# Performance work log

Hardware: AMD Instinct MI355X
Metric: run time of the kernel (lower is better)

The kernel has to match this reference:

```python
import jax, jax.numpy as jnp
import numpy as np

D_MODEL = 1024
NHEADS = 16
E_HEAD = D_MODEL // NHEADS  # 64
ROPE_BASE = 10000.0


def _rope_cos_sin(L, dim, base, dtype):
    # dim = E_head (even); inv_freq over pairs, GPT-NeoX half-split convention
    inv_freq = 1.0 / (base ** (jnp.arange(0, dim, 2, dtype=jnp.float32) / dim))
    pos = jnp.arange(L, dtype=jnp.float32)
    freqs = pos[:, None] * inv_freq[None, :]  # [L, dim/2]
    return jnp.cos(freqs).astype(dtype), jnp.sin(freqs).astype(dtype)


def _apply_rope(t, cos, sin):
    # t: [B, H, L, Dh]; rotate-half formulation
    d2 = t.shape[-1] // 2
    t1, t2 = t[..., :d2], t[..., d2:]
    return jnp.concatenate([t1 * cos - t2 * sin, t1 * sin + t2 * cos], axis=-1)


def setup_inputs() -> dict:
    key = jax.random.key(0)
    ks = jax.random.split(key, 5)
    B, L = 4, 2048
    x = jax.random.normal(ks[0], (B, L, D_MODEL), dtype=jnp.float32)
    s_in = 1.0 / np.sqrt(D_MODEL)
    W_packed = jax.random.normal(ks[1], (3 * D_MODEL, D_MODEL), dtype=jnp.float32) * s_in
    b_packed = jax.random.normal(ks[2], (3 * D_MODEL,), dtype=jnp.float32) * 0.02
    W_out = jax.random.normal(ks[3], (D_MODEL, D_MODEL), dtype=jnp.float32) * s_in
    b_out = jax.random.normal(ks[4], (D_MODEL,), dtype=jnp.float32) * 0.02
    return {"x": x, "W_packed": W_packed, "b_packed": b_packed, "W_out": W_out, "b_out": b_out}


def reference(x, W_packed, b_packed, W_out, b_out):
    B, L, _ = x.shape
    # 1) packed QKV projection (query is key is value path)
    qkv = jnp.einsum('ble,fe->blf', x, W_packed) + b_packed  # [B, L, 3*D]
    q, k, v = jnp.split(qkv, 3, axis=-1)
    # 2) split heads -> [B, H, L, Dh]
    def heads(t):
        return t.reshape(B, L, NHEADS, E_HEAD).transpose(0, 2, 1, 3)
    q, k, v = heads(q), heads(k), heads(v)
    # 3) RoPE on q, k
    cos, sin = _rope_cos_sin(L, E_HEAD, ROPE_BASE, x.dtype)
    q = _apply_rope(q, cos, sin)
    k = _apply_rope(k, cos, sin)
    # 4) SDPA (non-causal, no dropout)
    scale = 1.0 / np.sqrt(E_HEAD)
    scores = jnp.einsum('bhqd,bhkd->bhqk', q, k) * scale
    attn = jax.nn.softmax(scores, axis=-1)
    out = jnp.einsum('bhqk,bhkd->bhqd', attn, v)
    # 5) merge heads + output projection
    out = out.transpose(0, 2, 1, 3).reshape(B, L, D_MODEL)
    return jnp.einsum('bld,ed->ble', out, W_out) + b_out
```

## Files before the change

### kernel.cpp

```cpp
#include <hip/hip_runtime.h>
#include <hip/hip_bf16.h>
#include <stdint.h>

#define L_SEQ 2048
#define NB    4
#define NH    16
#define EH    64
#define DM    1024
#define MTOT  (NB * L_SEQ)

typedef __attribute__((ext_vector_type(8))) short bf16x8;
typedef __attribute__((ext_vector_type(4))) float f32x4;
typedef __attribute__((ext_vector_type(16))) float f32x16;
typedef __attribute__((ext_vector_type(2))) unsigned uint2v;

static __device__ __forceinline__ float bf2f(short u) {
    union { unsigned int i; float f; } c;
    c.i = ((unsigned int)(unsigned short)u) << 16;
    return c.f;
}
static __device__ __forceinline__ short f2bf(float f) {
    union { float f; unsigned int i; } c; c.f = f;
    unsigned int x = c.i;
    unsigned int r = (x + 0x7fffu + ((x >> 16) & 1u)) >> 16;
    return (short)(unsigned short)r;
}
static __device__ __forceinline__ unsigned cvtpk(float lo, float hi) {
    unsigned r;
    asm volatile("v_cvt_pk_bf16_f32 %0, %1, %2" : "=v"(r) : "v"(lo), "v"(hi));
    return r;
}
static __device__ __forceinline__ float pairsum(float x) {
    union { float f; unsigned u; } c; c.f = x;
    uint2v r = __builtin_amdgcn_permlane32_swap(c.u, c.u, false, false);
    union { unsigned u; float f; } a, b; a.u = r[0]; b.u = r[1];
    return a.f + b.f;
}

static __device__ __forceinline__ void gload_lds16(const void* g, void* lds) {
    __builtin_amdgcn_global_load_lds(
        (const __attribute__((address_space(1))) unsigned int*)g,
        (__attribute__((address_space(3))) unsigned int*)lds, 16, 0, 0);
}

__global__ __launch_bounds__(256) void cvt3_k(const float* __restrict__ x,
                                              const float* __restrict__ wp,
                                              const float* __restrict__ wo,
                                              short* __restrict__ xb,
                                              short* __restrict__ wpb,
                                              short* __restrict__ wob,
                                              float* __restrict__ tab) {
    int bid = blockIdx.x;
    if (bid >= 12288) {
        int i = (bid - 12288) * 256 + threadIdx.x;
        int l = i >> 5, d = i & 31;
        float inv = powf(10000.0f, -(float)d * (1.0f / 32.0f));
        float fr = (float)l * inv;
        tab[i]         = cosf(fr);
        tab[65536 + i] = sinf(fr);
        return;
    }
    const float* src; short* dst; int i;
    if (bid < 8192)       { src = x;  dst = xb;  i = bid * 256 + threadIdx.x; }
    else if (bid < 11264) { src = wp; dst = wpb; i = (bid - 8192) * 256 + threadIdx.x; }
    else                  { src = wo; dst = wob; i = (bid - 11264) * 256 + threadIdx.x; }
    float4 v = ((const float4*)src)[i];
    short4 o;
    o.x = f2bf(v.x); o.y = f2bf(v.y); o.z = f2bf(v.z); o.w = f2bf(v.w);
    ((short4*)dst)[i] = o;
}

template<int OUTBF16, int NBN, int NCOL, int EPI>
__global__ __launch_bounds__(512, 2) void gemmA_k(const short* __restrict__ A,
                                                  const short* __restrict__ Bt,
                                                  const float* __restrict__ bias,
                                                  void* __restrict__ Cv,
                                                  short* __restrict__ Qp,
                                                  short* __restrict__ Kp,
                                                  short* __restrict__ Vt,
                                                  const float* __restrict__ tab) {
    __shared__ short lds[3][384 * 32];
    const int t = threadIdx.x;
    const int w = t >> 6, l = t & 63;
    const int wm = w >> 1, wn = w & 1;
    const int lr = l & 15, lh = l >> 4;

    const int nblk = NBN * 32;
    int fid = blockIdx.x + blockIdx.y * NBN;
    int swz = (fid & 7) * (nblk >> 3) + (fid >> 3);
    const int n0 = (swz % NBN) * 128;
    const int m0 = (swz / NBN) * 256;

    const int lrow = l >> 2;
    const int schunk = (l & 3) ^ ((l >> 3) & 3);

    const short* Ag = A + (size_t)(m0 + lrow) * 1024 + schunk * 8;
    const short* Bg = Bt + (size_t)(n0 + lrow) * 1024 + schunk * 8;

    auto STAGE = [&](int kt, short* dst) {
        gload_lds16(Ag + (size_t)(w * 32) * 1024 + kt * 32,      dst + (w * 32) * 32);
        gload_lds16(Ag + (size_t)(w * 32 + 16) * 1024 + kt * 32, dst + (w * 32 + 16) * 32);
        gload_lds16(Bg + (size_t)(w * 16) * 1024 + kt * 32,      dst + 8192 + (w * 16) * 32);
    };

    f32x4 acc[4][4] = {};

    STAGE(0, &lds[0][0]);
    STAGE(1, &lds[1][0]);
    asm volatile("s_waitcnt vmcnt(3)" ::: "memory");
    __builtin_amdgcn_s_barrier();

    short* Pc = &lds[0][0];
    short* Pn = &lds[1][0];
    short* Pf = &lds[2][0];

    const int fch = (lh ^ ((lr >> 1) & 3)) << 3;

    for (int kt = 0; kt < 32; ++kt) {
        if (kt < 30) STAGE(kt + 2, Pf);

        const short* Al = Pc;
        const short* Bl = Pc + 8192;

        bf16x8 bfr[4], af[4];
#pragma unroll
        for (int nj = 0; nj < 4; ++nj)
            bfr[nj] = *(const bf16x8*)(Bl + (wn * 64 + nj * 16 + lr) * 32 + fch);
#pragma unroll
        for (int mi = 0; mi < 4; ++mi)
            af[mi] = *(const bf16x8*)(Al + (wm * 64 + mi * 16 + lr) * 32 + fch);

        __builtin_amdgcn_s_setprio(1);
#pragma unroll
        for (int mi = 0; mi < 4; ++mi)
#pragma unroll
            for (int nj = 0; nj < 4; ++nj)
                acc[mi][nj] = __builtin_amdgcn_mfma_f32_16x16x32_bf16(
                    af[mi], bfr[nj], acc[mi][nj], 0, 0, 0);
        __builtin_amdgcn_s_setprio(0);

        asm volatile("s_waitcnt lgkmcnt(0)" ::: "memory");
        if (kt < 30) asm volatile("s_waitcnt vmcnt(3)" ::: "memory");
        else         asm volatile("s_waitcnt vmcnt(0)" ::: "memory");
        __builtin_amdgcn_s_barrier();

        short* tp = Pc; Pc = Pn; Pn = Pf; Pf = tp;
    }

    if (EPI == 0) {
#pragma unroll
        for (int mi = 0; mi < 4; ++mi) {
#pragma unroll
            for (int nj = 0; nj < 4; ++nj) {
                const int row = m0 + wm * 64 + mi * 16 + lh * 4;
                const int col = n0 + wn * 64 + nj * 16 + lr;
                const float bsv = bias[col];
#pragma unroll
                for (int j = 0; j < 4; ++j) {
                    float v = acc[mi][nj][j] + bsv;
                    if (OUTBF16)
                        ((short*)Cv)[(size_t)(row + j) * NCOL + col] = f2bf(v);
                    else
                        ((float*)Cv)[(size_t)(row + j) * NCOL + col] = v;
                }
            }
        }
    } else {
        const int part = n0 >> 10;
        const int h = ((n0 & 1023) >> 6) + wn;
        if (part == 2) {
#pragma unroll
            for (int mi = 0; mi < 4; ++mi) {
                const int r0 = m0 + wm * 64 + mi * 16 + lh * 4;
                const int bq = r0 >> 11, lq = r0 & 2047;
                const int lpb = (lq & ~63) + (((mi * 2 + (lh & 1)) ^ (lr & 7)) << 3) + ((lh >> 1) * 4);
#pragma unroll
                for (int nj = 0; nj < 4; ++nj) {
                    const int d = nj * 16 + lr;
                    const float bsv = bias[n0 + wn * 64 + d];
                    short4 sv;
                    sv.x = f2bf(acc[mi][nj][0] + bsv);
                    sv.y = f2bf(acc[mi][nj][1] + bsv);
                    sv.z = f2bf(acc[mi][nj][2] + bsv);
                    sv.w = f2bf(acc[mi][nj][3] + bsv);
                    *(short4*)(Vt + (size_t)((bq * 16 + h) * 64 + d) * 2048 + lpb) = sv;
                }
            }
        } else {
            const float qsc = (part == 0) ? 0.18033688011112042f : 1.0f;
            short* Dst = (part == 0) ? Qp : Kp;
            const float b1l = bias[n0 + wn * 64 + lr];
            const float b1h = bias[n0 + wn * 64 + 16 + lr];
            const float b2l = bias[n0 + wn * 64 + 32 + lr];
            const float b2h = bias[n0 + wn * 64 + 48 + lr];
#pragma unroll
            for (int mi = 0; mi < 4; ++mi) {
                const int r0 = m0 + wm * 64 + mi * 16 + lh * 4;
                const int bq = r0 >> 11, lq0 = r0 & 2047;
                short* Drow = Dst + ((size_t)(bq * 16 + h) * 2048 + lq0) * 64;
#pragma unroll
                for (int j = 0; j < 4; ++j) {
                    const int ll = lq0 + j;
                    const int r7l = ll & 7;
#pragma unroll
                    for (int njl = 0; njl < 2; ++njl) {
                        const int d2 = njl * 16 + lr;
                        const float c = tab[ll * 32 + d2];
                        const float s = tab[65536 + ll * 32 + d2];
                        const float t1 = acc[mi][njl][j]     + (njl ? b1h : b1l);
                        const float t2 = acc[mi][njl + 2][j] + (njl ? b2h : b2l);
                        const float e1 = (t1 * c - t2 * s) * qsc;
                        const float e2 = (t1 * s + t2 * c) * qsc;
                        if (part == 0) {
                            Drow[j * 64 + d2]      = f2bf(e1);
                            Drow[j * 64 + d2 + 32] = f2bf(e2);
                        } else {
                            Drow[j * 64 + (((d2 >> 3) ^ r7l) * 8) + (d2 & 7)]       = f2bf(e1);
                            Drow[j * 64 + ((((d2 >> 3) | 4) ^ r7l) * 8) + (d2 & 7)] = f2bf(e2);
                        }
                    }
                }
            }
        }
    }
}

__global__ __launch_bounds__(512, 4) void attn_k(const short* __restrict__ Qg,
                                                 const short* __restrict__ Kg,
                                                 const short* __restrict__ Vt,
                                                 short* __restrict__ O) {
    __shared__ short Ks[3][64 * 64];
    __shared__ short Vs[3][64 * 64];
    const int t = threadIdx.x;
    const int w = t >> 6, l = t & 63;
    const int q = l & 31, hi = l >> 5;
    const int r7 = l & 7;

    const int od = blockIdx.x + blockIdx.y * 8;
    const int qblk = (od >> 3) & 7;
    const int bh = (od & 7) * 8 + (od >> 6);
    const int q0 = qblk * 256;

    const short* Qb = Qg + (size_t)bh * (2048 * 64);
    const short* Kb = Kg + (size_t)bh * (2048 * 64);
    const short* Vb = Vt + (size_t)bh * (64 * 2048);

    const int grow = w * 8 + (l >> 3);
    const int gcol = r7 * 8;

    gload_lds16(Kb + (size_t)grow * 64 + gcol,        &Ks[0][w * 512]);
    gload_lds16(Vb + (size_t)grow * 2048 + gcol,      &Vs[0][w * 512]);
    gload_lds16(Kb + (size_t)(64 + grow) * 64 + gcol, &Ks[1][w * 512]);
    gload_lds16(Vb + (size_t)grow * 2048 + 64 + gcol, &Vs[1][w * 512]);

    const int qrow = q0 + w * 32 + q;
    bf16x8 qf[4];
#pragma unroll
    for (int ds = 0; ds < 4; ds++)
        qf[ds] = *(const bf16x8*)(Qb + (size_t)qrow * 64 + ds * 16 + hi * 8);

    f32x16 o0 = {}, o1 = {};
    float lsumT = 0.0f;
    bf16x8 pf[4];

    asm volatile("s_waitcnt vmcnt(3)" ::: "memory");
    __builtin_amdgcn_s_barrier();

    {
        f32x16 s0 = {}, s1 = {};
#pragma unroll
        for (int ds = 0; ds < 4; ds++) {
            const int ch = ((ds << 1) | hi) ^ r7;
            bf16x8 k0f = *(const bf16x8*)(&Ks[0][0] + q * 64 + ch * 8);
            bf16x8 k1f = *(const bf16x8*)(&Ks[0][0] + (32 + q) * 64 + ch * 8);
            s0 = __builtin_amdgcn_mfma_f32_32x32x16_bf16(k0f, qf[ds], s0, 0, 0, 0);
            s1 = __builtin_amdgcn_mfma_f32_32x32x16_bf16(k1f, qf[ds], s1, 0, 0, 0);
        }
#pragma unroll
        for (int r = 0; r < 16; r++) {
            s0[r] = __builtin_amdgcn_exp2f(s0[r]);
            s1[r] = __builtin_amdgcn_exp2f(s1[r]);
        }
        float ts[16];
#pragma unroll
        for (int r = 0; r < 16; r++) ts[r] = s0[r] + s1[r];
#pragma unroll
        for (int st = 8; st >= 1; st >>= 1)
#pragma unroll
            for (int i = 0; i < 8; i++) if (i < st) ts[i] = ts[i] + ts[i + st];
        lsumT += pairsum(ts[0]);
        union { unsigned u[4]; bf16x8 v; } f;
        f.u[0] = cvtpk(s0[0], s0[1]);  f.u[1] = cvtpk(s0[2], s0[3]);
        f.u[2] = cvtpk(s0[4], s0[5]);  f.u[3] = cvtpk(s0[6], s0[7]);
        pf[0] = f.v;
        f.u[0] = cvtpk(s0[8], s0[9]);  f.u[1] = cvtpk(s0[10], s0[11]);
        f.u[2] = cvtpk(s0[12], s0[13]); f.u[3] = cvtpk(s0[14], s0[15]);
        pf[1] = f.v;
        f.u[0] = cvtpk(s1[0], s1[1]);  f.u[1] = cvtpk(s1[2], s1[3]);
        f.u[2] = cvtpk(s1[4], s1[5]);  f.u[3] = cvtpk(s1[6], s1[7]);
        pf[2] = f.v;
        f.u[0] = cvtpk(s1[8], s1[9]);  f.u[1] = cvtpk(s1[10], s1[11]);
        f.u[2] = cvtpk(s1[12], s1[13]); f.u[3] = cvtpk(s1[14], s1[15]);
        pf[3] = f.v;
    }

    asm volatile("s_waitcnt vmcnt(1)" ::: "memory");
    __builtin_amdgcn_s_barrier();

    const short* Kc = &Ks[0][0];  const short* Vc = &Vs[0][0];
    const short* Kn = &Ks[1][0];  const short* Vn = &Vs[1][0];
    short*       Kf = &Ks[2][0];  short*       Vf = &Vs[2][0];

    for (int it = 0; it < 32; ++it) {
        if (it < 30) {
            const int kn = (it + 2) * 64;
            gload_lds16(Kb + (size_t)(kn + grow) * 64 + gcol, Kf + w * 512);
            gload_lds16(Vb + (size_t)grow * 2048 + kn + gcol, Vf + w * 512);
        }

        f32x16 s0 = {}, s1 = {};
#pragma unroll
        for (int ks = 0; ks < 4; ks++) {
            const int ch = ((ks << 1) | hi) ^ r7;
            bf16x8 v0f = *(const bf16x8*)(Vc + q * 64 + ch * 8);
            bf16x8 v1f = *(const bf16x8*)(Vc + (32 + q) * 64 + ch * 8);
            __builtin_amdgcn_s_setprio(1);
            o0 = __builtin_amdgcn_mfma_f32_32x32x16_bf16(v0f, pf[ks], o0, 0, 0, 0);
            o1 = __builtin_amdgcn_mfma_f32_32x32x16_bf16(v1f, pf[ks], o1, 0, 0, 0);
            __builtin_amdgcn_s_setprio(0);
            if (it < 31) {
                bf16x8 k0f = *(const bf16x8*)(Kn + q * 64 + ch * 8);
                bf16x8 k1f = *(const bf16x8*)(Kn + (32 + q) * 64 + ch * 8);
                __builtin_amdgcn_s_setprio(1);
                s0 = __builtin_amdgcn_mfma_f32_32x32x16_bf16(k0f, qf[ks], s0, 0, 0, 0);
                s1 = __builtin_amdgcn_mfma_f32_32x32x16_bf16(k1f, qf[ks], s1, 0, 0, 0);
                __builtin_amdgcn_s_setprio(0);
            }
        }

        if (it < 31) {
#pragma unroll
            for (int r = 0; r < 16; r++) {
                s0[r] = __builtin_amdgcn_exp2f(s0[r]);
                s1[r] = __builtin_amdgcn_exp2f(s1[r]);
            }
            float ts[16];
#pragma unroll
            for (int r = 0; r < 16; r++) ts[r] = s0[r] + s1[r];
#pragma unroll
            for (int st = 8; st >= 1; st >>= 1)
#pragma unroll
                for (int i = 0; i < 8; i++) if (i < st) ts[i] = ts[i] + ts[i + st];
            lsumT += pairsum(ts[0]);
            union { unsigned u[4]; bf16x8 v; } f;
            f.u[0] = cvtpk(s0[0], s0[1]);  f.u[1] = cvtpk(s0[2], s0[3]);
            f.u[2] = cvtpk(s0[4], s0[5]);  f.u[3] = cvtpk(s0[6], s0[7]);
            pf[0] = f.v;
            f.u[0] = cvtpk(s0[8], s0[9]);  f.u[1] = cvtpk(s0[10], s0[11]);
            f.u[2] = cvtpk(s0[12], s0[13]); f.u[3] = cvtpk(s0[14], s0[15]);
            pf[1] = f.v;
            f.u[0] = cvtpk(s1[0], s1[1]);  f.u[1] = cvtpk(s1[2], s1[3]);
            f.u[2] = cvtpk(s1[4], s1[5]);  f.u[3] = cvtpk(s1[6], s1[7]);
            pf[2] = f.v;
            f.u[0] = cvtpk(s1[8], s1[9]);  f.u[1] = cvtpk(s1[10], s1[11]);
            f.u[2] = cvtpk(s1[12], s1[13]); f.u[3] = cvtpk(s1[14], s1[15]);
            pf[3] = f.v;
        }

        asm volatile("s_waitcnt lgkmcnt(0)" ::: "memory");
        if (it < 30) asm volatile("s_waitcnt vmcnt(1)" ::: "memory");
        else         asm volatile("s_waitcnt vmcnt(0)" ::: "memory");
        __builtin_amdgcn_s_barrier();

        const short* tk = Kc; Kc = Kn; Kn = Kf; Kf = (short*)tk;
        const short* tv = Vc; Vc = Vn; Vn = Vf; Vf = (short*)tv;
    }

    const float inv = 1.0f / lsumT;
    const int b = bh >> 4, h = bh & 15;
    short* Orow = O + (size_t)(b * 2048 + qrow) * 1024 + h * 64;
#pragma unroll
    for (int g = 0; g < 4; g++) {
        unsigned w0 = cvtpk(o0[g * 4 + 0] * inv, o0[g * 4 + 1] * inv);
        unsigned w1 = cvtpk(o0[g * 4 + 2] * inv, o0[g * 4 + 3] * inv);
        unsigned long long p0 = (unsigned long long)w0 | ((unsigned long long)w1 << 32);
        *(unsigned long long*)(Orow + g * 8 + hi * 4) = p0;
        unsigned w2 = cvtpk(o1[g * 4 + 0] * inv, o1[g * 4 + 1] * inv);
        unsigned w3 = cvtpk(o1[g * 4 + 2] * inv, o1[g * 4 + 3] * inv);
        unsigned long long p1 = (unsigned long long)w2 | ((unsigned long long)w3 << 32);
        *(unsigned long long*)(Orow + 32 + g * 8 + hi * 4) = p1;
    }
}

extern "C" void kernel_launch(void* const* d_in, const int* in_sizes, int n_in,
                              void* d_out, int out_size, void* d_ws, size_t ws_size,
                              hipStream_t stream) {
    const float* x  = (const float*)d_in[0];
    const float* Wp = (const float*)d_in[1];
    const float* bp = (const float*)d_in[2];
    const float* Wo = (const float*)d_in[3];
    const float* bo = (const float*)d_in[4];

    char* ws = (char*)d_ws;
    const size_t SZ_XB  = (size_t)MTOT * DM * 2;
    const size_t SZ_WPB = (size_t)3 * DM * DM * 2;
    const size_t SZ_WOB = (size_t)DM * DM * 2;
    const size_t SZ_BHLE = (size_t)MTOT * DM * 2;

    short* xb   = (short*)(ws);
    short* wpb  = (short*)(ws + SZ_XB);
    short* wob  = (short*)(ws + SZ_XB + SZ_WPB);
    short* Qb   = (short*)(ws + SZ_XB + SZ_WPB + SZ_WOB);
    short* Kb   = (short*)(ws + SZ_XB + SZ_WPB + SZ_WOB + SZ_BHLE);
    short* Vtb  = (short*)(ws + SZ_XB + SZ_WPB + SZ_WOB + 2 * SZ_BHLE);
    short* Ob   = (short*)(ws + SZ_XB + SZ_WPB + SZ_WOB + 3 * SZ_BHLE);
    float* tab  = (float*)(ws + SZ_XB + SZ_WPB + SZ_WOB + 4 * SZ_BHLE);

    cvt3_k<<<12544, 256, 0, stream>>>(x, Wp, Wo, xb, wpb, wob, tab);

    gemmA_k<1, 24, 3072, 1><<<dim3(24, 32), 512, 0, stream>>>(
        xb, wpb, bp, nullptr, Qb, Kb, Vtb, tab);

    attn_k<<<dim3(8, 64), 512, 0, stream>>>(Qb, Kb, Vtb, Ob);

    gemmA_k<0, 8, 1024, 0><<<dim3(8, 32), 512, 0, stream>>>(
        Ob, wob, bo, (float*)d_out, nullptr, nullptr, nullptr, nullptr);
}
```

Before: 176.8 us.

## Deepen attention K/V prefetch ring and halve barriers by processing two tiles per sync

The attention kernel's triple-buffered K/V shared-memory ring becomes a 4-slot K and 5-slot V ring, with three tiles preloaded. The main loop now issues two tile prefetches and runs two KV iterations per barrier, which halves the number of block-wide syncs. Waiting on all loads (vmcnt(0)) at each barrier means prefetch distance varies between one and two iterations. Shared memory per block grows from 48KB to 72KB, which may lower occupancy against the requested 4 blocks per CU.

```diff
diff --git a/kernel.cpp b/kernel.cpp
--- a/kernel.cpp
+++ b/kernel.cpp
@@ -229,8 +229,8 @@
                                                  const short* __restrict__ Kg,
                                                  const short* __restrict__ Vt,
                                                  short* __restrict__ O) {
-    __shared__ short Ks[3][64 * 64];
-    __shared__ short Vs[3][64 * 64];
+    __shared__ short Ks[4][64 * 64];
+    __shared__ short Vs[5][64 * 64];
     const int t = threadIdx.x;
     const int w = t >> 6, l = t & 63;
     const int q = l & 31, hi = l >> 5;
@@ -245,25 +245,27 @@
     const short* Kb = Kg + (size_t)bh * (2048 * 64);
     const short* Vb = Vt + (size_t)bh * (64 * 2048);
 
+    const int qrow = q0 + w * 32 + q;
+    bf16x8 qf[4];
+#pragma unroll
+    for (int ds = 0; ds < 4; ds++)
+        qf[ds] = *(const bf16x8*)(Qb + (size_t)qrow * 64 + ds * 16 + hi * 8);
+
     const int grow = w * 8 + (l >> 3);
     const int gcol = r7 * 8;
 
-    gload_lds16(Kb + (size_t)grow * 64 + gcol,        &Ks[0][w * 512]);
-    gload_lds16(Vb + (size_t)grow * 2048 + gcol,      &Vs[0][w * 512]);
-    gload_lds16(Kb + (size_t)(64 + grow) * 64 + gcol, &Ks[1][w * 512]);
-    gload_lds16(Vb + (size_t)grow * 2048 + 64 + gcol, &Vs[1][w * 512]);
-
-    const int qrow = q0 + w * 32 + q;
-    bf16x8 qf[4];
-#pragma unroll
-    for (int ds = 0; ds < 4; ds++)
-        qf[ds] = *(const bf16x8*)(Qb + (size_t)qrow * 64 + ds * 16 + hi * 8);
+    gload_lds16(Kb + (size_t)grow * 64 + gcol,          &Ks[0][w * 512]);
+    gload_lds16(Vb + (size_t)grow * 2048 + gcol,        &Vs[0][w * 512]);
+    gload_lds16(Kb + (size_t)(64 + grow) * 64 + gcol,   &Ks[1][w * 512]);
+    gload_lds16(Vb + (size_t)grow * 2048 + 64 + gcol,   &Vs[1][w * 512]);
+    gload_lds16(Kb + (size_t)(128 + grow) * 64 + gcol,  &Ks[2][w * 512]);
+    gload_lds16(Vb + (size_t)grow * 2048 + 128 + gcol,  &Vs[2][w * 512]);
 
     f32x16 o0 = {}, o1 = {};
     float lsumT = 0.0f;
     bf16x8 pf[4];
 
-    asm volatile("s_waitcnt vmcnt(3)" ::: "memory");
+    asm volatile("s_waitcnt vmcnt(5)" ::: "memory");
     __builtin_amdgcn_s_barrier();
 
     {
@@ -304,20 +306,13 @@
         pf[3] = f.v;
     }
 
-    asm volatile("s_waitcnt vmcnt(1)" ::: "memory");
+    asm volatile("s_waitcnt lgkmcnt(0)" ::: "memory");
+    asm volatile("s_waitcnt vmcnt(0)" ::: "memory");
     __builtin_amdgcn_s_barrier();
 
-    const short* Kc = &Ks[0][0];  const short* Vc = &Vs[0][0];
-    const short* Kn = &Ks[1][0];  const short* Vn = &Vs[1][0];
-    short*       Kf = &Ks[2][0];  short*       Vf = &Vs[2][0];
-
-    for (int it = 0; it < 32; ++it) {
-        if (it < 30) {
-            const int kn = (it + 2) * 64;
-            gload_lds16(Kb + (size_t)(kn + grow) * 64 + gcol, Kf + w * 512);
-            gload_lds16(Vb + (size_t)grow * 2048 + kn + gcol, Vf + w * 512);
-        }
-
+    auto ITER = [&](int it) {
+        const short* Vc = &Vs[it % 5][0];
+        const short* Kn = &Ks[(it + 1) & 3][0];
         f32x16 s0 = {}, s1 = {};
 #pragma unroll
         for (int ks = 0; ks < 4; ks++) {
@@ -337,7 +332,6 @@
                 __builtin_amdgcn_s_setprio(0);
             }
         }
-
         if (it < 31) {
 #pragma unroll
             for (int r = 0; r < 16; r++) {
@@ -366,14 +360,25 @@
             f.u[2] = cvtpk(s1[12], s1[13]); f.u[3] = cvtpk(s1[14], s1[15]);
             pf[3] = f.v;
         }
+    };
+
+    for (int P = 0; P < 16; ++P) {
+        const int t3 = 2 * P + 3, t4 = 2 * P + 4;
+        if (t3 < 32) {
+            gload_lds16(Kb + (size_t)(t3 * 64 + grow) * 64 + gcol, &Ks[t3 & 3][w * 512]);
+            gload_lds16(Vb + (size_t)grow * 2048 + t3 * 64 + gcol, &Vs[t3 % 5][w * 512]);
+        }
+        if (t4 < 32) {
+            gload_lds16(Kb + (size_t)(t4 * 64 + grow) * 64 + gcol, &Ks[t4 & 3][w * 512]);
+            gload_lds16(Vb + (size_t)grow * 2048 + t4 * 64 + gcol, &Vs[t4 % 5][w * 512]);
+        }
+
+        ITER(2 * P);
+        ITER(2 * P + 1);
 
         asm volatile("s_waitcnt lgkmcnt(0)" ::: "memory");
-        if (it < 30) asm volatile("s_waitcnt vmcnt(1)" ::: "memory");
-        else         asm volatile("s_waitcnt vmcnt(0)" ::: "memory");
+        asm volatile("s_waitcnt vmcnt(0)" ::: "memory");
         __builtin_amdgcn_s_barrier();
-
-        const short* tk = Kc; Kc = Kn; Kn = Kf; Kf = (short*)tk;
-        const short* tv = Vc; Vc = Vn; Vn = Vf; Vf = (short*)tv;
     }
 
     const float inv = 1.0f / lsumT;
```

Result: no change. 178.9 us (+1.2%).
